# Optimization experiments

Measured on AMD Instinct MI355X. Metric: run time of the kernel, lower is better.

The kernel has to match this reference:

```python
import jax, jax.numpy as jnp
import numpy as np

N = 50000      # nodes
E = 500000     # edges (before self-loops)
IN = 128       # input_channels
HID = 64       # hidden_channels
HEADS = 4
OUT = 10       # output_channels
G = 64         # number of graphs in batch


def setup_inputs() -> dict:
    key = jax.random.key(0)
    ks = jax.random.split(key, 12)
    x = jax.random.normal(ks[0], (N, IN), jnp.float32)
    edge_index = jax.random.randint(ks[1], (2, E), 0, N, jnp.int32)
    edge_weight = jax.random.uniform(ks[2], (E,), jnp.float32)
    batch = jnp.sort(jax.random.randint(ks[3], (N,), 0, G, jnp.int32))
    # GATConv layer 1: heads=4, concat=True
    W1 = jax.random.normal(ks[4], (HEADS * HID, IN), jnp.float32) / np.sqrt(IN)
    att_src1 = jax.random.normal(ks[5], (1, HEADS, HID), jnp.float32) / np.sqrt(HID)
    att_dst1 = jax.random.normal(ks[6], (1, HEADS, HID), jnp.float32) / np.sqrt(HID)
    b1 = jnp.zeros((HEADS * HID,), jnp.float32)
    # GATConv layer 2: heads=1, concat=False
    W2 = jax.random.normal(ks[7], (OUT, HEADS * HID), jnp.float32) / np.sqrt(HEADS * HID)
    att_src2 = jax.random.normal(ks[8], (1, 1, OUT), jnp.float32) / np.sqrt(OUT)
    att_dst2 = jax.random.normal(ks[9], (1, 1, OUT), jnp.float32) / np.sqrt(OUT)
    b2 = jnp.zeros((OUT,), jnp.float32)
    return {"x": x, "edge_index": edge_index, "edge_weight": edge_weight, "batch": batch,
            "W1": W1, "att_src1": att_src1, "att_dst1": att_dst1, "b1": b1,
            "W2": W2, "att_src2": att_src2, "att_dst2": att_dst2, "b2": b2}


def _gat_layer(x, src, dst, W, a_src, a_dst, heads, ch, n):
    # x: [n, in] -> h: [n, heads, ch]
    h = (x @ W.T).reshape(n, heads, ch)
    alpha_s = (h * a_src).sum(-1)  # [n, heads]
    alpha_d = (h * a_dst).sum(-1)
    e = jax.nn.leaky_relu(alpha_s[src] + alpha_d[dst], 0.2)  # [E', heads]
    # segment softmax over incoming edges of each destination node
    emax = jax.ops.segment_max(e, dst, num_segments=n)
    emax = jnp.where(jnp.isfinite(emax), emax, 0.0)
    ee = jnp.exp(e - emax[dst])
    denom = jax.ops.segment_sum(ee, dst, num_segments=n)
    alpha = ee / (denom[dst] + 1e-16)
    # weighted scatter-add of source features
    return jax.ops.segment_sum(alpha[:, :, None] * h[src], dst, num_segments=n)


def reference(x, edge_index, edge_weight, batch, W1, att_src1, att_dst1, b1,
              W2, att_src2, att_dst2, b2):
    # eval mode: dropout inactive; edge_weight is ignored by GATConv (as in source)
    n = x.shape[0]
    loops = jnp.arange(n, dtype=edge_index.dtype)  # PyG add_self_loops=True
    src = jnp.concatenate([edge_index[0], loops])
    dst = jnp.concatenate([edge_index[1], loops])
    h1 = _gat_layer(x, src, dst, W1, att_src1, att_dst1, HEADS, HID, n)
    h1 = jax.nn.elu(h1.reshape(n, HEADS * HID) + b1)
    h2 = _gat_layer(h1, src, dst, W2, att_src2, att_dst2, 1, OUT, n)[:, 0, :] + b2
    # global mean pool over graphs
    counts = jax.ops.segment_sum(jnp.ones((n,), h2.dtype), batch, num_segments=G)
    pooled = jax.ops.segment_sum(h2, batch, num_segments=G) / jnp.maximum(counts, 1.0)[:, None]
    return jax.nn.log_softmax(pooled, axis=1)
```

## Files before the change

### kernel.cpp

```cpp
#include <hip/hip_runtime.h>
#include <hip/hip_bf16.h>
#include <math.h>

#define NN 50000
#define EE 500000
#define ETOT (EE + NN)
#define NG 64

typedef __attribute__((ext_vector_type(8))) short short8v;
typedef __attribute__((ext_vector_type(4))) float float4v;
typedef __attribute__((ext_vector_type(2))) float float2v;

__device__ __forceinline__ float bf2f(unsigned short u) {
    unsigned int v = ((unsigned int)u) << 16;
    return __builtin_bit_cast(float, v);
}
__device__ __forceinline__ unsigned short f2bf(float f) {
    __hip_bfloat16 h = __float2bfloat16(f);
    return *(unsigned short*)&h;
}

__global__ void k_prep(uint4* __restrict__ zp, int n16, int zB,
                       const float* __restrict__ W1, unsigned short* __restrict__ wb,
                       const float* __restrict__ x, unsigned short* __restrict__ xb) {
    int b = blockIdx.x;
    if (b < zB) {
        int t = b * 256 + threadIdx.x;
        if (t < n16) zp[t] = make_uint4(0, 0, 0, 0);
    } else if (b < zB + 128) {
        int t = (b - zB) * 256 + threadIdx.x;
        wb[t] = f2bf(W1[t]);
    } else {
        int t = (b - zB - 128) * 256 + threadIdx.x;
        if (t < NN * 128 / 8) {
            float4 a = *(const float4*)&x[(size_t)t * 8];
            float4 c = *(const float4*)&x[(size_t)t * 8 + 4];
            float f[8] = {a.x, a.y, a.z, a.w, c.x, c.y, c.z, c.w};
            short8v vh;
#pragma unroll
            for (int j = 0; j < 8; ++j) vh[j] = (short)f2bf(f[j]);
            *(short8v*)&xb[(size_t)t * 8] = vh;
        }
    }
}

__global__ __launch_bounds__(256) void k_big(int gemmB, int gE,
                                             const int* __restrict__ ei,
                                             const int* __restrict__ batch,
                                             int* __restrict__ counts,
                                             int* __restrict__ ord,
                                             int* __restrict__ gcount,
                                             const unsigned short* __restrict__ xb,
                                             const unsigned short* __restrict__ wb,
                                             const float* __restrict__ att_s,
                                             const float* __restrict__ att_d,
                                             unsigned char* __restrict__ h1f8,
                                             float* __restrict__ alpha_s,
                                             float* __restrict__ alpha_d) {
    int bx = (int)blockIdx.x;
    bool isHist;
    int idx;
    if (bx < 2 * gemmB) {
        isHist = !(bx & 1);
        idx = bx >> 1;
    } else {
        isHist = true;
        idx = bx - gemmB;
    }
    if (isHist) {
        int t = idx * 256 + threadIdx.x;
        if (t < ETOT) {
            int dst = (t < EE) ? ei[EE + t] : (t - EE);
            ord[t] = atomicAdd(counts + dst, 1);
        }
        if (t < NN) {
            int g = batch[t];
            int g0 = __shfl(g, 0);
            bool same = (g == g0);
            unsigned long long m = __ballot(same);
            if (same) {
                if ((threadIdx.x & 63) == (__ffsll((long long)m) - 1))
                    atomicAdd(gcount + g0, (int)__popcll(m));
            } else {
                atomicAdd(gcount + g, 1);
            }
        }
        return;
    }
    int w = threadIdx.x >> 6;
    int l = threadIdx.x & 63;
    int bm0 = idx * 32;
    int i16 = l & 15;
    int kb = (l >> 4) * 8;
    int colb = w * 64;

    short8v a[2][4];
#pragma unroll
    for (int mi = 0; mi < 2; ++mi) {
        int r = bm0 + mi * 16 + i16;
#pragma unroll
        for (int k = 0; k < 4; ++k) {
            if (r < NN) a[mi][k] = *(const short8v*)&xb[(size_t)r * 128 + k * 32 + kb];
            else        a[mi][k] = (short8v){0,0,0,0,0,0,0,0};
        }
    }

    float4v acc[2][4];
#pragma unroll
    for (int mi = 0; mi < 2; ++mi)
#pragma unroll
        for (int ni = 0; ni < 4; ++ni)
            acc[mi][ni] = (float4v){0.f, 0.f, 0.f, 0.f};

#pragma unroll
    for (int k = 0; k < 4; ++k) {
#pragma unroll
        for (int ni = 0; ni < 4; ++ni) {
            short8v b = *(const short8v*)&wb[(size_t)(colb + ni * 16 + i16) * 128 + k * 32 + kb];
            acc[0][ni] = __builtin_amdgcn_mfma_f32_16x16x32_bf16(a[0][k], b, acc[0][ni], 0, 0, 0);
            acc[1][ni] = __builtin_amdgcn_mfma_f32_16x16x32_bf16(a[1][k], b, acc[1][ni], 0, 0, 0);
        }
    }

    int drb = (l >> 4) * 4;
    int dc = l & 15;
    float asw[4], adw[4];
#pragma unroll
    for (int ni = 0; ni < 4; ++ni) {
        asw[ni] = att_s[colb + ni * 16 + dc];
        adw[ni] = att_d[colb + ni * 16 + dc];
    }
#pragma unroll
    for (int mi = 0; mi < 2; ++mi) {
#pragma unroll
        for (int r = 0; r < 4; ++r) {
            int row = bm0 + mi * 16 + drb + r;
            float v0 = acc[mi][0][r], v1 = acc[mi][1][r];
            float v2 = acc[mi][2][r], v3 = acc[mi][3][r];
            float s = v0 * asw[0] + v1 * asw[1] + v2 * asw[2] + v3 * asw[3];
            float d = v0 * adw[0] + v1 * adw[1] + v2 * adw[2] + v3 * adw[3];
            unsigned int packed = __builtin_amdgcn_cvt_pk_fp8_f32(v0, v1, 0u, false);
            packed = __builtin_amdgcn_cvt_pk_fp8_f32(v2, v3, packed, true);
            if (row < NN)
                *(unsigned int*)&h1f8[((unsigned)row << 8) + (unsigned)(colb + (dc << 2))] = packed;
#pragma unroll
            for (int m = 8; m >= 1; m >>= 1) {
                s += __shfl_xor(s, m);
                d += __shfl_xor(d, m);
            }
            if (dc == 0 && row < NN) {
                alpha_s[row * 4 + w] = s;
                alpha_d[row * 4 + w] = d;
            }
        }
    }
}

__global__ void k_scan(const int* __restrict__ counts, int* __restrict__ indptr) {
    __shared__ int wsum[16];
    __shared__ int carry_s;
    int tid = threadIdx.x;
    int lane = tid & 63;
    int w = tid >> 6;
    int4 v[13];
#pragma unroll
    for (int c = 0; c < 13; ++c) {
        int i = c * 4096 + tid * 4;
        if (i + 3 < NN) {
            v[c] = *(const int4*)&counts[i];
        } else {
            v[c] = make_int4(0, 0, 0, 0);
            if (i < NN) v[c].x = counts[i];
            if (i + 1 < NN) v[c].y = counts[i + 1];
            if (i + 2 < NN) v[c].z = counts[i + 2];
        }
    }
    if (tid == 0) carry_s = 0;
    __syncthreads();
#pragma unroll
    for (int c = 0; c < 13; ++c) {
        int i = c * 4096 + tid * 4;
        int v0 = v[c].x, v1 = v[c].y, v2 = v[c].z, v3 = v[c].w;
        int tot = v0 + v1 + v2 + v3;
        int s = tot;
#pragma unroll
        for (int off = 1; off < 64; off <<= 1) {
            int u = __shfl_up(s, off);
            if (lane >= off) s += u;
        }
        if (lane == 63) wsum[w] = s;
        __syncthreads();
        if (w == 0) {
            int t2 = (lane < 16) ? wsum[lane] : 0;
#pragma unroll
            for (int off = 1; off < 16; off <<= 1) {
                int u = __shfl_up(t2, off);
                if (lane >= off) t2 += u;
            }
            if (lane < 16) wsum[lane] = t2;
        }
        __syncthreads();
        int wpre = (w == 0) ? 0 : wsum[w - 1];
        int incl = s + wpre;
        int carry = carry_s;
        int e = carry + incl - tot;
        if (i < NN)     indptr[i] = e;
        if (i + 1 < NN) indptr[i + 1] = e + v0;
        if (i + 2 < NN) indptr[i + 2] = e + v0 + v1;
        if (i + 3 < NN) indptr[i + 3] = e + v0 + v1 + v2;
        __syncthreads();
        if (tid == 1023) carry_s = carry + incl;
        __syncthreads();
    }
    if (tid == 0) indptr[NN] = carry_s;
}

__global__ void k_fill(const int* __restrict__ ei, const int* __restrict__ indptr,
                       const int* __restrict__ ord,
                       const float* __restrict__ als, const float* __restrict__ ald,
                       uint4* __restrict__ edges, int* __restrict__ srcs) {
    int t = blockIdx.x * 256 + threadIdx.x;
    if (t >= ETOT) return;
    int src = (t < EE) ? ei[t] : (t - EE);
    int dst = (t < EE) ? ei[EE + t] : (t - EE);
    int p = indptr[dst] + ord[t];
    float4 as = *(const float4*)&als[src * 4];
    float4 ad = *(const float4*)&ald[dst * 4];
    float e0 = as.x + ad.x, e1 = as.y + ad.y, e2 = as.z + ad.z, e3 = as.w + ad.w;
    e0 = e0 > 0.f ? e0 : 0.2f * e0;
    e1 = e1 > 0.f ? e1 : 0.2f * e1;
    e2 = e2 > 0.f ? e2 : 0.2f * e2;
    e3 = e3 > 0.f ? e3 : 0.2f * e3;
    unsigned int ee01 = (unsigned int)f2bf(__expf(e0)) | ((unsigned int)f2bf(__expf(e1)) << 16);
    unsigned int ee23 = (unsigned int)f2bf(__expf(e2)) | ((unsigned int)f2bf(__expf(e3)) << 16);
    edges[p] = make_uint4((unsigned int)src, ee01, ee23, (unsigned int)dst);
    srcs[p] = src;
}

__global__ void k_gather1(const int* __restrict__ indptr, const uint4* __restrict__ edges,
                          const unsigned char* __restrict__ h1f8, const float* __restrict__ b1,
                          const float* __restrict__ W2, const float* __restrict__ as2v,
                          const float* __restrict__ ad2v, float* __restrict__ h2lin,
                          float* __restrict__ als2, float* __restrict__ ald2) {
    int wid = (blockIdx.x * 256 + threadIdx.x) >> 6;
    int l = threadIdx.x & 63;
    if (wid >= NN) return;
    int p0 = __builtin_amdgcn_readfirstlane(indptr[wid]);
    int p1 = __builtin_amdgcn_readfirstlane(indptr[wid + 1]);
    int last = p1 - 1;
    int head = l >> 4;
    unsigned sel = (head == 0) ? 0x01000C0Cu : (head == 1) ? 0x03020C0Cu
                 : (head == 2) ? 0x05040C0Cu : 0x07060C0Cu;
    unsigned lofs = (unsigned)(l << 2);
    float2v accA = {0.f, 0.f}, accB = {0.f, 0.f};
    float dsum = 0.f;
    for (int p = p0; p < p1; p += 8) {
        uint4 e[8];
#pragma unroll
        for (int j = 0; j < 8; ++j) {
            int idx = p + j;
            e[j] = edges[idx < p1 ? idx : last];
        }
        unsigned int hv[8];
#pragma unroll
        for (int j = 0; j < 8; ++j)
            hv[j] = *(const unsigned int*)(h1f8 + (((unsigned)e[j].x << 8) | lofs));
#pragma unroll
        for (int j = 0; j < 8; ++j) {
#if __has_builtin(__builtin_amdgcn_perm)
            unsigned wu = __builtin_amdgcn_perm(e[j].z, e[j].y, sel);
#else
            unsigned packed = (head & 2) ? e[j].z : e[j].y;
            unsigned wu = (head & 1) ? (packed & 0xffff0000u) : (packed << 16);
#endif
            float wgt = __builtin_bit_cast(float, wu);
            wgt = (p + j < p1) ? wgt : 0.f;
            float2v lo = __builtin_amdgcn_cvt_pk_f32_fp8(hv[j], false);
            float2v hi = __builtin_amdgcn_cvt_pk_f32_fp8(hv[j], true);
            float2v w2 = {wgt, wgt};
            accA += w2 * lo;
            accB += w2 * hi;
            dsum += wgt;
        }
    }
    float inv = 1.0f / dsum;
    int cbase = head * 64 + (l & 15);
    float o0 = accA[0] * inv + b1[cbase];
    float o1 = accA[1] * inv + b1[cbase + 16];
    float o2 = accB[0] * inv + b1[cbase + 32];
    float o3 = accB[1] * inv + b1[cbase + 48];
    o0 = o0 > 0.f ? o0 : (__expf(o0) - 1.0f);
    o1 = o1 > 0.f ? o1 : (__expf(o1) - 1.0f);
    o2 = o2 > 0.f ? o2 : (__expf(o2) - 1.0f);
    o3 = o3 > 0.f ? o3 : (__expf(o3) - 1.0f);
    float t[10];
#pragma unroll
    for (int o = 0; o < 10; ++o) {
        const float* wr = &W2[o * 256 + cbase];
        t[o] = o0 * wr[0] + o1 * wr[16] + o2 * wr[32] + o3 * wr[48];
    }
#pragma unroll
    for (int m = 32; m > 0; m >>= 1) {
#pragma unroll
        for (int o = 0; o < 10; ++o) t[o] += __shfl_xor(t[o], m);
    }
    if (l == 0) {
        float as = 0.f, ad = 0.f;
#pragma unroll
        for (int o = 0; o < 10; ++o) {
            h2lin[(size_t)wid * 16 + o] = t[o];
            as += t[o] * as2v[o];
            ad += t[o] * ad2v[o];
        }
        als2[wid] = as;
        ald2[wid] = ad;
    }
}

__global__ void k_g2pool(const int* __restrict__ indptr, const int* __restrict__ srcs,
                         const float* __restrict__ als2, const float* __restrict__ ald2,
                         const float* __restrict__ h2lin, const float* __restrict__ b2,
                         const int* __restrict__ batch, float* __restrict__ pooled) {
    int wave = (blockIdx.x * 256 + threadIdx.x) >> 6;
    int lane = threadIdx.x & 63;
    int grp = lane >> 4, c = lane & 15;
    int node = wave * 4 + grp;
    float acc = 0.f;
    int g = -1;
    if (node < NN) {
        int p0 = indptr[node], p1 = indptr[node + 1];
        int last = p1 - 1;
        float ad2n = ald2[node];
        float dsum = 0.f;
        for (int p = p0; p < p1; p += 4) {
            int i1 = p + 1, i2 = p + 2, i3 = p + 3;
            unsigned s0 = (unsigned)srcs[p];
            unsigned s1 = (unsigned)srcs[i1 < p1 ? i1 : last];
            unsigned s2 = (unsigned)srcs[i2 < p1 ? i2 : last];
            unsigned s3 = (unsigned)srcs[i3 < p1 ? i3 : last];
            float v0 = als2[s0] + ad2n;
            float v1 = als2[s1] + ad2n;
            float v2 = als2[s2] + ad2n;
            float v3 = als2[s3] + ad2n;
            float h0 = 0.f, h1_ = 0.f, h2 = 0.f, h3 = 0.f;
            if (c < 10) {
                h0 = h2lin[(s0 << 4) + (unsigned)c];
                h1_ = h2lin[(s1 << 4) + (unsigned)c];
                h2 = h2lin[(s2 << 4) + (unsigned)c];
                h3 = h2lin[(s3 << 4) + (unsigned)c];
            }
            v0 = v0 > 0.f ? v0 : 0.2f * v0;
            v1 = v1 > 0.f ? v1 : 0.2f * v1;
            v2 = v2 > 0.f ? v2 : 0.2f * v2;
            v3 = v3 > 0.f ? v3 : 0.2f * v3;
            float w0 = __expf(v0);
            float w1 = (i1 < p1) ? __expf(v1) : 0.f;
            float w2 = (i2 < p1) ? __expf(v2) : 0.f;
            float w3 = (i3 < p1) ? __expf(v3) : 0.f;
            dsum += (w0 + w1) + (w2 + w3);
            acc += w0 * h0 + w1 * h1_ + w2 * h2 + w3 * h3;
        }
        if (c < 10) acc = acc / dsum + b2[c];
        else acc = 0.f;
        g = batch[node];
    }
    int g0 = __shfl(g, 0);
    bool uni = __all((node >= NN) || (g == g0));
    if (uni) {
        if (g0 >= 0) {
            acc += __shfl_xor(acc, 16);
            acc += __shfl_xor(acc, 32);
            if (grp == 0 && c < 10)
                atomicAdd(pooled + g0 * 10 + c, acc);
        }
    } else if (node < NN && c < 10) {
        atomicAdd(pooled + g * 10 + c, acc);
    }
}

__global__ void k_final(const float* __restrict__ pooled, const int* __restrict__ gcount,
                        float* __restrict__ out) {
    int g = threadIdx.x;
    if (g >= NG) return;
    float c = fmaxf((float)gcount[g], 1.0f);
    float m[10];
    float mx = -1e30f;
#pragma unroll
    for (int i = 0; i < 10; ++i) {
        m[i] = pooled[g * 10 + i] / c;
        mx = fmaxf(mx, m[i]);
    }
    float s = 0.f;
#pragma unroll
    for (int i = 0; i < 10; ++i) s += expf(m[i] - mx);
    float lse = mx + logf(s);
#pragma unroll
    for (int i = 0; i < 10; ++i) out[g * 10 + i] = m[i] - lse;
}

extern "C" void kernel_launch(void* const* d_in, const int* in_sizes, int n_in,
                              void* d_out, int out_size, void* d_ws, size_t ws_size,
                              hipStream_t stream) {
    const float* x   = (const float*)d_in[0];
    const int*   ei  = (const int*)d_in[1];
    const int*   bat = (const int*)d_in[3];
    const float* W1  = (const float*)d_in[4];
    const float* as1 = (const float*)d_in[5];
    const float* ad1 = (const float*)d_in[6];
    const float* b1  = (const float*)d_in[7];
    const float* W2  = (const float*)d_in[8];
    const float* as2 = (const float*)d_in[9];
    const float* ad2 = (const float*)d_in[10];
    const float* b2  = (const float*)d_in[11];
    float* out = (float*)d_out;

    char* ws = (char*)d_ws;
    size_t off = 0;
    auto alloc = [&](size_t bytes) -> size_t {
        size_t o = off;
        off = (off + bytes + 255) & ~(size_t)255;
        return o;
    };
    size_t o_counts = alloc((size_t)NN * 4);
    size_t o_pooled = alloc((size_t)NG * 10 * 4);
    size_t o_gcount = alloc((size_t)NG * 4);
    size_t zero_bytes = off;
    size_t o_ord    = alloc((size_t)ETOT * 4);
    size_t o_indptr = alloc((size_t)(NN + 1) * 4);
    size_t o_edges  = alloc((size_t)ETOT * 16);
    size_t o_srcs   = alloc((size_t)ETOT * 4);
    size_t o_h1f8   = alloc((size_t)NN * 256);
    size_t o_als1   = alloc((size_t)NN * 4 * 4);
    size_t o_ald1   = alloc((size_t)NN * 4 * 4);
    size_t o_h2lin  = alloc((size_t)NN * 16 * 4);
    size_t o_als2   = alloc((size_t)NN * 4);
    size_t o_ald2   = alloc((size_t)NN * 4);
    size_t o_wb     = alloc((size_t)256 * 128 * 2);
    size_t o_xb     = alloc((size_t)NN * 128 * 2);
    (void)ws_size;

    int*   counts = (int*)(ws + o_counts);
    float* pooled = (float*)(ws + o_pooled);
    int*   gcount = (int*)(ws + o_gcount);
    int*   ord    = (int*)(ws + o_ord);
    int*   indptr = (int*)(ws + o_indptr);
    uint4* edges  = (uint4*)(ws + o_edges);
    int*   srcs   = (int*)(ws + o_srcs);
    unsigned char*  h1f8 = (unsigned char*)(ws + o_h1f8);
    float* als1   = (float*)(ws + o_als1);
    float* ald1   = (float*)(ws + o_ald1);
    float* h2lin  = (float*)(ws + o_h2lin);
    float* als2   = (float*)(ws + o_als2);
    float* ald2   = (float*)(ws + o_ald2);
    unsigned short* wb = (unsigned short*)(ws + o_wb);
    unsigned short* xb = (unsigned short*)(ws + o_xb);

    int n16 = (int)(zero_bytes / 16);
    int zB = (n16 + 255) / 256;
    int xB = (NN * 128 / 8 + 255) / 256;
    int gE = (ETOT + 255) / 256;
    int gW = (NN + 3) / 4;
    int gemmB = (NN + 31) / 32;

    k_prep<<<zB + 128 + xB, 256, 0, stream>>>((uint4*)ws, n16, zB, W1, wb, x, xb);
    k_big<<<gE + gemmB, 256, 0, stream>>>(gemmB, gE, ei, bat, counts, ord, gcount,
                                          xb, wb, as1, ad1, h1f8, als1, ald1);
    k_scan<<<1, 1024, 0, stream>>>(counts, indptr);
    k_fill<<<gE, 256, 0, stream>>>(ei, indptr, ord, als1, ald1, edges, srcs);
    k_gather1<<<gW, 256, 0, stream>>>(indptr, edges, h1f8, b1, W2, as2, ad2,
                                      h2lin, als2, ald2);
    k_g2pool<<<gW, 256, 0, stream>>>(indptr, srcs, als2, ald2, h2lin, b2, bat, pooled);
    k_final<<<1, 64, 0, stream>>>(pooled, gcount, out);
    (void)n_in; (void)in_sizes; (void)out_size;
}
```

Baseline: 164.0 us.

## Split degree histogram into eight partitions to cut atomic contention

The destination-degree histogram is split into eight partitioned count arrays, chosen by block index, so concurrent atomics on the same node spread across copies. The scan kernel merges the partitions, turns them into per-partition exclusive offsets and writes those back, and the fill kernel adds the partition offset when placing each edge. This aims to reduce atomic serialization in the histogram, at the cost of eight times the zeroing work, more scan-kernel memory traffic in a single-block kernel, and an extra gather in the fill kernel.

Result: slower. 192.8 us (+17.5%).

```diff
diff --git a/kernel.cpp b/kernel.cpp
--- a/kernel.cpp
+++ b/kernel.cpp
@@ -47,7 +47,7 @@
 __global__ __launch_bounds__(256) void k_big(int gemmB, int gE,
                                              const int* __restrict__ ei,
                                              const int* __restrict__ batch,
-                                             int* __restrict__ counts,
+                                             int* __restrict__ counts8,
                                              int* __restrict__ ord,
                                              int* __restrict__ gcount,
                                              const unsigned short* __restrict__ xb,
@@ -68,10 +68,11 @@
         idx = bx - gemmB;
     }
     if (isHist) {
+        int part = bx & 7;
         int t = idx * 256 + threadIdx.x;
         if (t < ETOT) {
             int dst = (t < EE) ? ei[EE + t] : (t - EE);
-            ord[t] = atomicAdd(counts + dst, 1);
+            ord[t] = atomicAdd(counts8 + part * NN + dst, 1);
         }
         if (t < NN) {
             int g = batch[t];
@@ -156,31 +157,43 @@
     }
 }
 
-__global__ void k_scan(const int* __restrict__ counts, int* __restrict__ indptr) {
+__global__ void k_scan(int* __restrict__ counts8, int* __restrict__ indptr) {
     __shared__ int wsum[16];
     __shared__ int carry_s;
     int tid = threadIdx.x;
     int lane = tid & 63;
     int w = tid >> 6;
-    int4 v[13];
-#pragma unroll
+    if (tid == 0) carry_s = 0;
+    __syncthreads();
     for (int c = 0; c < 13; ++c) {
         int i = c * 4096 + tid * 4;
-        if (i + 3 < NN) {
-            v[c] = *(const int4*)&counts[i];
-        } else {
-            v[c] = make_int4(0, 0, 0, 0);
-            if (i < NN) v[c].x = counts[i];
-            if (i + 1 < NN) v[c].y = counts[i + 1];
-            if (i + 2 < NN) v[c].z = counts[i + 2];
-        }
-    }
-    if (tid == 0) carry_s = 0;
-    __syncthreads();
-#pragma unroll
-    for (int c = 0; c < 13; ++c) {
-        int i = c * 4096 + tid * 4;
-        int v0 = v[c].x, v1 = v[c].y, v2 = v[c].z, v3 = v[c].w;
+        bool full = (i + 3 < NN);
+        int4 q[8];
+#pragma unroll
+        for (int p = 0; p < 8; ++p) {
+            if (full) {
+                q[p] = *(const int4*)&counts8[p * NN + i];
+            } else {
+                q[p] = make_int4(0, 0, 0, 0);
+                if (i < NN) q[p].x = counts8[p * NN + i];
+                if (i + 1 < NN) q[p].y = counts8[p * NN + i + 1];
+                if (i + 2 < NN) q[p].z = counts8[p * NN + i + 2];
+            }
+        }
+        int4 pre = make_int4(0, 0, 0, 0);
+#pragma unroll
+        for (int p = 0; p < 8; ++p) {
+            int4 cur = q[p];
+            if (full) {
+                *(int4*)&counts8[p * NN + i] = pre;
+            } else {
+                if (i < NN) counts8[p * NN + i] = pre.x;
+                if (i + 1 < NN) counts8[p * NN + i + 1] = pre.y;
+                if (i + 2 < NN) counts8[p * NN + i + 2] = pre.z;
+            }
+            pre.x += cur.x; pre.y += cur.y; pre.z += cur.z; pre.w += cur.w;
+        }
+        int v0 = pre.x, v1 = pre.y, v2 = pre.z, v3 = pre.w;
         int tot = v0 + v1 + v2 + v3;
         int s = tot;
 #pragma unroll
@@ -215,7 +228,8 @@
     if (tid == 0) indptr[NN] = carry_s;
 }
 
-__global__ void k_fill(const int* __restrict__ ei, const int* __restrict__ indptr,
+__global__ void k_fill(int gemmB, const int* __restrict__ ei,
+                       const int* __restrict__ indptr, const int* __restrict__ counts8,
                        const int* __restrict__ ord,
                        const float* __restrict__ als, const float* __restrict__ ald,
                        uint4* __restrict__ edges, int* __restrict__ srcs) {
@@ -223,7 +237,10 @@
     if (t >= ETOT) return;
     int src = (t < EE) ? ei[t] : (t - EE);
     int dst = (t < EE) ? ei[EE + t] : (t - EE);
-    int p = indptr[dst] + ord[t];
+    int idx = t >> 8;
+    int bxp = (idx < gemmB) ? (idx << 1) : (idx + gemmB);
+    int part = bxp & 7;
+    int p = indptr[dst] + counts8[part * NN + dst] + ord[t];
     float4 as = *(const float4*)&als[src * 4];
     float4 ad = *(const float4*)&ald[dst * 4];
     float e0 = as.x + ad.x, e1 = as.y + ad.y, e2 = as.z + ad.z, e3 = as.w + ad.w;
@@ -421,9 +438,9 @@
         off = (off + bytes + 255) & ~(size_t)255;
         return o;
     };
-    size_t o_counts = alloc((size_t)NN * 4);
-    size_t o_pooled = alloc((size_t)NG * 10 * 4);
-    size_t o_gcount = alloc((size_t)NG * 4);
+    size_t o_counts8 = alloc((size_t)8 * NN * 4);
+    size_t o_pooled  = alloc((size_t)NG * 10 * 4);
+    size_t o_gcount  = alloc((size_t)NG * 4);
     size_t zero_bytes = off;
     size_t o_ord    = alloc((size_t)ETOT * 4);
     size_t o_indptr = alloc((size_t)(NN + 1) * 4);
@@ -439,19 +456,19 @@
     size_t o_xb     = alloc((size_t)NN * 128 * 2);
     (void)ws_size;
 
-    int*   counts = (int*)(ws + o_counts);
-    float* pooled = (float*)(ws + o_pooled);
-    int*   gcount = (int*)(ws + o_gcount);
-    int*   ord    = (int*)(ws + o_ord);
-    int*   indptr = (int*)(ws + o_indptr);
-    uint4* edges  = (uint4*)(ws + o_edges);
-    int*   srcs   = (int*)(ws + o_srcs);
+    int*   counts8 = (int*)(ws + o_counts8);
+    float* pooled  = (float*)(ws + o_pooled);
+    int*   gcount  = (int*)(ws + o_gcount);
+    int*   ord     = (int*)(ws + o_ord);
+    int*   indptr  = (int*)(ws + o_indptr);
+    uint4* edges   = (uint4*)(ws + o_edges);
+    int*   srcs    = (int*)(ws + o_srcs);
     unsigned char*  h1f8 = (unsigned char*)(ws + o_h1f8);
-    float* als1   = (float*)(ws + o_als1);
-    float* ald1   = (float*)(ws + o_ald1);
-    float* h2lin  = (float*)(ws + o_h2lin);
-    float* als2   = (float*)(ws + o_als2);
-    float* ald2   = (float*)(ws + o_ald2);
+    float* als1    = (float*)(ws + o_als1);
+    float* ald1    = (float*)(ws + o_ald1);
+    float* h2lin   = (float*)(ws + o_h2lin);
+    float* als2    = (float*)(ws + o_als2);
+    float* ald2    = (float*)(ws + o_ald2);
     unsigned short* wb = (unsigned short*)(ws + o_wb);
     unsigned short* xb = (unsigned short*)(ws + o_xb);
 
@@ -463,10 +480,11 @@
     int gemmB = (NN + 31) / 32;
 
     k_prep<<<zB + 128 + xB, 256, 0, stream>>>((uint4*)ws, n16, zB, W1, wb, x, xb);
-    k_big<<<gE + gemmB, 256, 0, stream>>>(gemmB, gE, ei, bat, counts, ord, gcount,
+    k_big<<<gE + gemmB, 256, 0, stream>>>(gemmB, gE, ei, bat, counts8, ord, gcount,
                                           xb, wb, as1, ad1, h1f8, als1, ald1);
-    k_scan<<<1, 1024, 0, stream>>>(counts, indptr);
-    k_fill<<<gE, 256, 0, stream>>>(ei, indptr, ord, als1, ald1, edges, srcs);
+    k_scan<<<1, 1024, 0, stream>>>(counts8, indptr);
+    k_fill<<<gE, 256, 0, stream>>>(gemmB, ei, indptr, counts8, ord, als1, ald1,
+                                   edges, srcs);
     k_gather1<<<gW, 256, 0, stream>>>(indptr, edges, h1f8, b1, W2, as2, ad2,
                                       h2lin, als2, ald2);
     k_g2pool<<<gW, 256, 0, stream>>>(indptr, srcs, als2, ald2, h2lin, b2, bat, pooled);
```
